# Optimization experiments

Hardware: AMD Instinct MI355X
Metric: run time of the kernel (lower is better)

## Reference

```python
import jax, jax.numpy as jnp
import numpy as np
import math

B, S, E, H, L = 32, 512, 256, 8, 2
Dh = E // H
NUM_Q, NUM_C, MAX_POS, R = 10000, 200, 512, 4


def setup_inputs() -> dict:
    key = jax.random.key(0)
    ks = jax.random.split(key, 32)
    f = lambda k, sh: (jax.random.normal(k, sh, jnp.float32) * 0.05)
    que_emb = f(ks[0], (NUM_Q + 1, E)).at[0].set(0.0)  # padding_idx=0
    inp = dict(
        pid_data=jax.random.randint(ks[1], (B, S), 0, NUM_Q + 1),
        c_data=jax.random.randint(ks[2], (B, S, R), 0, NUM_C),
        target=jax.random.randint(ks[3], (B, S), 0, 2),
        que_emb=que_emb,
        concept_emb=f(ks[4], (NUM_C, E)),
        pos_key_emb=f(ks[5], (MAX_POS, Dh)),
        pos_value_emb=f(ks[6], (MAX_POS, Dh)),
        qc_W=f(ks[7], (2 * E, E)), qc_b=jnp.zeros((E,), jnp.float32),
        lin_W=f(ks[8], (2 * E, E)), lin_b=jnp.zeros((E,), jnp.float32),
        Wq=f(ks[9], (L, E, E)), bq=jnp.zeros((L, E), jnp.float32),
        Wk=f(ks[10], (L, E, E)), bk=jnp.zeros((L, E), jnp.float32),
        Wv=f(ks[11], (L, E, E)), bv=jnp.zeros((L, E), jnp.float32),
        o1_W=f(ks[12], (2 * E, E)), o1_b=jnp.zeros((E,), jnp.float32),
        o2_W=f(ks[13], (E, E)), o2_b=jnp.zeros((E,), jnp.float32),
        o3_W=f(ks[14], (E, 1)), o3_b=jnp.zeros((1,), jnp.float32),
    )
    return inp


def _relative_attention(q_in, v_in, Wq, bq, Wk, bk, Wv, bv, pos_key_emb, pos_value_emb):
    b, s, e = q_in.shape
    proj = lambda x, W, bias: (x @ W + bias).reshape(b, s, H, Dh).transpose(0, 2, 1, 3)
    q = proj(q_in, Wq, bq)  # [b,h,s,dh]
    k = proj(q_in, Wk, bk)
    v = proj(v_in, Wv, bv)
    # relative position indices, clamped (Shaw et al. variant)
    i = jnp.arange(s)
    idxs = jnp.clip(i[:, None] - i[None, :], 0, MAX_POS - 1)  # [s,s]
    pos_k = pos_key_emb[idxs]    # [s,s,dh]
    pos_v = pos_value_emb[idxs]  # [s,s,dh]
    scores = jnp.einsum('bhid,bhjd->bhij', q, k) + jnp.einsum('bhid,ijd->bhij', q, pos_k)
    scores = scores / math.sqrt(Dh)
    # future_mask: triu with k=0 -> mask j >= i (incl. diagonal)
    causal = (i[None, :] >= i[:, None])  # [s,s] True where masked
    scores = jnp.where(causal, jnp.float32(-1e9), scores)
    p = jax.nn.softmax(scores, axis=-1)  # [b,h,i,j]
    # pad-zero trick: row i=0 of attention replaced by zeros
    p = p * (i[:, None] > 0).astype(p.dtype)
    # value = v + per-pair positional value bias
    out = jnp.einsum('bhij,bhjd->bhid', p, v) + jnp.einsum('bhij,ijd->bhid', p, pos_v)
    return out.transpose(0, 2, 1, 3).reshape(b, s, E), p


def reference(pid_data, c_data, target, que_emb, concept_emb, pos_key_emb,
              pos_value_emb, qc_W, qc_b, lin_W, lin_b, Wq, bq, Wk, bk, Wv, bv,
              o1_W, o1_b, o2_W, o2_b, o3_W, o3_b):
    qemb = que_emb[pid_data]  # [B,S,E]
    # average skill embedding; index 0 of padded table is the zero/pad row
    concept_cat = jnp.concatenate([jnp.zeros((1, E), concept_emb.dtype), concept_emb], axis=0)
    related = c_data + 1  # [B,S,R]
    cemb_sum = concept_cat[related].sum(axis=-2)  # [B,S,E]
    cnt = (related != 0).sum(axis=-1, keepdims=True)
    cnt = jnp.maximum(cnt, 1)
    cemb = cemb_sum / cnt.astype(cemb_sum.dtype)
    query = jnp.concatenate([qemb, cemb], axis=-1) @ qc_W + qc_b  # [B,S,E]
    # interaction embedding gated by response label
    lbl = target[..., None].astype(query.dtype)
    inter = jnp.concatenate([query * lbl, query * (1.0 - lbl)], axis=-1)
    inter = jax.nn.relu(inter @ lin_W + lin_b)  # [B,S,E]
    sim = jax.nn.sigmoid(jnp.einsum('bse,ce->bsc', qemb, concept_emb))
    outputs, _ = _relative_attention(query, inter, Wq[0], bq[0], Wk[0], bk[0],
                                     Wv[0], bv[0], pos_key_emb, pos_value_emb)
    for l in range(1, L):
        residual, _ = _relative_attention(outputs, inter, Wq[l], bq[l], Wk[l], bk[l],
                                          Wv[l], bv[l], pos_key_emb, pos_value_emb)
        outputs = outputs + jax.nn.relu(residual)
    h = jnp.concatenate([outputs, query], axis=-1)
    h = jax.nn.relu(h @ o1_W + o1_b)
    h = jax.nn.relu(h @ o2_W + o2_b)
    pred = jax.nn.sigmoid((h @ o3_W + o3_b).squeeze(-1))  # [B,S]
    return pred, sim
```

## Files before the change

### kernel.cpp

```cpp
#include <hip/hip_runtime.h>
#include <hip/hip_bf16.h>
#include <cmath>

#define B_   32
#define S_   512
#define E_   256
#define H_   8
#define DH_  32
#define L_   2
#define R_   4
#define NUMC_ 200
#define MAXPOS_ 512
#define MTOK (B_ * S_)

typedef __attribute__((ext_vector_type(8))) short bf16x8_t;
typedef __attribute__((ext_vector_type(4))) float f32x4_t;

__device__ inline ushort bfu(float a) {
    union { __hip_bfloat16 h; ushort u; } x; x.h = __float2bfloat16(a); return x.u;
}
__device__ inline uint pk2bf(float a, float b) {
    return (uint)bfu(a) | ((uint)bfu(b) << 16);
}
__device__ inline float bf2f(ushort u) {
    union { float f; uint u; } x; x.u = (uint)u << 16; return x.f;
}
__device__ inline __hip_bfloat16 f2bf(float a) { return __float2bfloat16(a); }

__global__ __launch_bounds__(256) void wcvt_k(
    const float* __restrict__ qcW, const float* __restrict__ linW,
    const float* __restrict__ Wq, const float* __restrict__ Wk,
    const float* __restrict__ Wv, const float* __restrict__ o1W,
    const float* __restrict__ o2W, const float* __restrict__ ce,
    __hip_bfloat16* __restrict__ wb)
{
    int i = blockIdx.x * 256 + threadIdx.x;
    float v;
    if (i < 131072) {
        int n = i >> 9, k = i & 511; v = qcW[k * 256 + n];
    } else if (i < 262144) {
        int l = i - 131072; int n = l >> 9, k = l & 511; v = linW[k * 256 + n];
    } else if (i < 524288) {
        int l2 = i - 262144; int ly = l2 >> 17; int r2 = l2 & 131071;
        int n = r2 >> 8, k = r2 & 255;
        v = (n < 256) ? Wq[ly * 65536 + k * 256 + n]
                      : Wk[ly * 65536 + k * 256 + (n - 256)];
    } else if (i < 655360) {
        int l2 = i - 524288; int n = l2 >> 8, k = l2 & 255;
        int ly = n >> 8, nn = n & 255;
        v = Wv[ly * 65536 + k * 256 + nn];
    } else if (i < 786432) {
        int l = i - 655360; int n = l >> 9, k = l & 511; v = o1W[k * 256 + n];
    } else if (i < 851968) {
        int l = i - 786432; int n = l >> 8, k = l & 255; v = o2W[k * 256 + n];
    } else {
        int l = i - 851968; int c = l >> 8, k = l & 255;
        v = (c < NUMC_) ? ce[c * 256 + k] : 0.f;
    }
    wb[i] = f2bf(v);
}

__global__ __launch_bounds__(256) void embed_k(
    const int* __restrict__ pid, const int* __restrict__ cdat,
    const float* __restrict__ qe, const float* __restrict__ ce,
    __hip_bfloat16* __restrict__ qemb, __hip_bfloat16* __restrict__ cemb)
{
    int tkn = blockIdx.x;
    int e   = threadIdx.x;
    int p = pid[tkn];
    qemb[(size_t)tkn * E_ + e] = f2bf(qe[(size_t)p * E_ + e]);
    const int* c = cdat + (size_t)tkn * R_;
    float s = 0.f;
#pragma unroll
    for (int r = 0; r < R_; ++r) s += ce[(size_t)c[r] * E_ + e];
    cemb[(size_t)tkn * E_ + e] = f2bf(s * 0.25f);
}

template<int AMODE, int EPI, int OMODE, int K, int NB>
__global__ __launch_bounds__(256) void gemm_bf_k(
    const __hip_bfloat16* __restrict__ A0, const __hip_bfloat16* __restrict__ A1,
    const int* __restrict__ lbl,
    const __hip_bfloat16* __restrict__ BT,
    const float* __restrict__ bias, const float* __restrict__ bias2,
    void* __restrict__ C0, void* __restrict__ C1, int Nstride)
{
    const int lane = threadIdx.x & 63, w = threadIdx.x >> 6;
    const int col = lane & 15, rg = lane >> 4;
    const int wr = w >> 1, wc = w & 1;
    int did = blockIdx.y * gridDim.x + blockIdx.x;
    int bm, bn;
    if (NB == 512) {
        int swz = (did & 7) * 128 + (did >> 3);
        bm = (swz >> 2) * 64; bn = (swz & 3) * 128;
    } else {
        int swz = (did & 7) * 64 + (did >> 3);
        bm = (swz >> 1) * 64; bn = (swz & 1) * 128;
    }
    const f32x4_t z4 = {0.f, 0.f, 0.f, 0.f};
    f32x4_t acc[2][4] = {{z4, z4, z4, z4}, {z4, z4, z4, z4}};
    const bf16x8_t z8 = {0, 0, 0, 0, 0, 0, 0, 0};

    int rowA[2];
    rowA[0] = bm + wr * 32 + col;
    rowA[1] = bm + wr * 32 + 16 + col;
    int lblv[2] = {0, 0};
    if (AMODE == 2) { lblv[0] = lbl[rowA[0]]; lblv[1] = lbl[rowA[1]]; }
    const int nb0 = bn + wc * 64;

    for (int k0 = 0; k0 < K; k0 += 32) {
        const int kk = k0 + 8 * rg;
        bf16x8_t af[2], bfr[4];
#pragma unroll
        for (int mt = 0; mt < 2; ++mt) {
            if (AMODE == 0) {
                af[mt] = *reinterpret_cast<const bf16x8_t*>(A0 + (size_t)rowA[mt] * K + kk);
            } else if (AMODE == 1) {
                const __hip_bfloat16* p = (kk < 256) ? (A0 + (size_t)rowA[mt] * 256 + kk)
                                                     : (A1 + (size_t)rowA[mt] * 256 + (kk - 256));
                af[mt] = *reinterpret_cast<const bf16x8_t*>(p);
            } else {
                bf16x8_t a = *reinterpret_cast<const bf16x8_t*>(A0 + (size_t)rowA[mt] * 256 + (kk & 255));
                bool first = (kk < 256);
                af[mt] = ((lblv[mt] != 0) == first) ? a : z8;
            }
        }
#pragma unroll
        for (int nt = 0; nt < 4; ++nt)
            bfr[nt] = *reinterpret_cast<const bf16x8_t*>(BT + (size_t)(nb0 + nt * 16 + col) * K + kk);

        __builtin_amdgcn_s_setprio(1);
#pragma unroll
        for (int mt = 0; mt < 2; ++mt)
#pragma unroll
        for (int nt = 0; nt < 4; ++nt)
            acc[mt][nt] = __builtin_amdgcn_mfma_f32_16x16x32_bf16(af[mt], bfr[nt], acc[mt][nt], 0, 0, 0);
        __builtin_amdgcn_s_setprio(0);
    }

#pragma unroll
    for (int mt = 0; mt < 2; ++mt)
#pragma unroll
    for (int nt = 0; nt < 4; ++nt) {
        const int n = nb0 + nt * 16 + col;
        const int mb = bm + wr * 32 + mt * 16 + 4 * rg;
        float bs = 0.f;
        if (bias) bs = (NB == 512 && n >= 256) ? bias2[n - 256] : bias[n];
        float xv[4];
#pragma unroll
        for (int r = 0; r < 4; ++r) {
            float x = acc[mt][nt][r] + bs;
            if (EPI == 1) x = fmaxf(x, 0.f);
            else if (EPI == 2) x = 1.f / (1.f + expf(-x));
            xv[r] = x;
        }
        if (OMODE == 0) {
            if (n < Nstride) {
                float* C = (float*)C0;
#pragma unroll
                for (int r = 0; r < 4; ++r)
                    C[(size_t)(mb + r) * Nstride + n] = xv[r];
            }
        } else if (OMODE == 3) {
            __hip_bfloat16* Cb = (__hip_bfloat16*)C0;
#pragma unroll
            for (int r = 0; r < 4; ++r)
                Cb[(size_t)(mb + r) * 256 + n] = f2bf(xv[r]);
        } else if (OMODE == 1) {
            __hip_bfloat16* dst = (n < 256) ? (__hip_bfloat16*)C0 : (__hip_bfloat16*)C1;
            const int nn = n & 255, hh = nn >> 5, d = nn & 31;
#pragma unroll
            for (int r = 0; r < 4; ++r) {
                int m = mb + r;
                int bh = (m >> 9) * 8 + hh;
                dst[((size_t)bh * 512 + (m & 511)) * 32 + d] = f2bf(xv[r]);
            }
        } else {
            __hip_bfloat16* dst = (n < 256) ? (__hip_bfloat16*)C0 : (__hip_bfloat16*)C1;
            const int nn = n & 255, hh = nn >> 5, d = nn & 31;
            const int bh = (mb >> 9) * 8 + hh;
            ushort4 pk;
            pk.x = bfu(xv[0]); pk.y = bfu(xv[1]); pk.z = bfu(xv[2]); pk.w = bfu(xv[3]);
            *reinterpret_cast<ushort4*>(dst + ((size_t)bh * 32 + d) * 512 + (mb & 511)) = pk;
        }
    }
}

__global__ __launch_bounds__(256) void poscvt_k(
    const float* __restrict__ posk, const float* __restrict__ posv,
    __hip_bfloat16* __restrict__ pkPad, __hip_bfloat16* __restrict__ pvT)
{
    int t = blockIdx.x * 256 + threadIdx.x;
    {
        int row = t >> 5, d = t & 31;
        int rel = row - 32;
        float v = (rel >= 0 && rel < MAXPOS_) ? posk[(size_t)rel * DH_ + d] : 0.f;
        pkPad[t] = f2bf(v);
    }
    {
        int d = t / 576, c = t - d * 576;
        int rel = c - 31;
        float v = (rel >= 0 && rel < MAXPOS_) ? posv[(size_t)rel * DH_ + d] : 0.f;
        pvT[t] = f2bf(v);
    }
}

#define QPST 38
template<int ADDREL>
__global__ __launch_bounds__(256) void attn_mfma_k(
    const __hip_bfloat16* __restrict__ Qbf, const __hip_bfloat16* __restrict__ Kbf,
    const __hip_bfloat16* __restrict__ Vt,  const __hip_bfloat16* __restrict__ pkPad,
    const __hip_bfloat16* __restrict__ pvT, __hip_bfloat16* __restrict__ outp)
{
    __shared__ __align__(16) ushort ldsA_s[4][64 * QPST];
    __shared__ __align__(16) ushort ldsP_s[4][2304];

    const int w = threadIdx.x >> 6, lane = threadIdx.x & 63;
    const int col = lane & 15, rg = lane >> 4;
    const int bh = blockIdx.x, b = bh >> 3, h = bh & 7;
    const int s = blockIdx.y * 4 + w;
    const int band = (s & 1) ? (15 - (s >> 1)) : (s >> 1);
    const int i0 = band * 32;

    ushort* ldsA = ldsA_s[w];
    ushort* ldsP = ldsP_s[w];

    {
        uint4 zz = make_uint4(0u, 0u, 0u, 0u);
        uint4* pz = reinterpret_cast<uint4*>(ldsP);
#pragma unroll
        for (int t = 0; t < 5; ++t) {
            int idx = lane + 64 * t;
            if (idx < 288) pz[idx] = zz;
        }
    }

    const __hip_bfloat16* Qb = Qbf + (size_t)bh * 512 * 32;
    const __hip_bfloat16* Kb = Kbf + (size_t)bh * 512 * 32;
    const __hip_bfloat16* Vb = Vt  + (size_t)bh * 32 * 512;

    bf16x8_t qf[2];
    qf[0] = *reinterpret_cast<const bf16x8_t*>(Qb + (size_t)(i0 + col) * 32 + 8 * rg);
    qf[1] = *reinterpret_cast<const bf16x8_t*>(Qb + (size_t)(i0 + 16 + col) * 32 + 8 * rg);

    const f32x4_t z4 = {0.f, 0.f, 0.f, 0.f};
    f32x4_t o[2][2] = {{z4, z4}, {z4, z4}};
    float lrow[2][4] = {};
    const float rscale = 0.17677669529663687f;

    for (int j0 = 0; j0 <= i0; j0 += 32) {
        bf16x8_t kf0 = *reinterpret_cast<const bf16x8_t*>(Kb + (size_t)(j0 + col) * 32 + 8 * rg);
        bf16x8_t kf1 = *reinterpret_cast<const bf16x8_t*>(Kb + (size_t)(j0 + 16 + col) * 32 + 8 * rg);
        const int prow0 = i0 - j0 + 1;
        bf16x8_t pkf[4];
#pragma unroll
        for (int rt = 0; rt < 4; ++rt)
            pkf[rt] = *reinterpret_cast<const bf16x8_t*>(
                pkPad + (size_t)(prow0 + rt * 16 + col) * 32 + 8 * rg);

        __builtin_amdgcn_s_setprio(1);
        f32x4_t sA[2][2];
        sA[0][0] = __builtin_amdgcn_mfma_f32_16x16x32_bf16(qf[0], kf0, z4, 0, 0, 0);
        sA[0][1] = __builtin_amdgcn_mfma_f32_16x16x32_bf16(qf[0], kf1, z4, 0, 0, 0);
        sA[1][0] = __builtin_amdgcn_mfma_f32_16x16x32_bf16(qf[1], kf0, z4, 0, 0, 0);
        sA[1][1] = __builtin_amdgcn_mfma_f32_16x16x32_bf16(qf[1], kf1, z4, 0, 0, 0);
        f32x4_t qp0[4], qp1[4];
#pragma unroll
        for (int rt = 0; rt < 4; ++rt) {
            qp0[rt] = __builtin_amdgcn_mfma_f32_16x16x32_bf16(qf[0], pkf[rt], z4, 0, 0, 0);
            qp1[rt] = __builtin_amdgcn_mfma_f32_16x16x32_bf16(qf[1], pkf[rt], z4, 0, 0, 0);
        }
        __builtin_amdgcn_s_setprio(0);

#pragma unroll
        for (int rt = 0; rt < 4; ++rt) {
            int xo = (rt * 16 + col) * QPST;
            uint2 wv;
            wv.x = pk2bf(qp0[rt][0], qp0[rt][1]);
            wv.y = pk2bf(qp0[rt][2], qp0[rt][3]);
            *reinterpret_cast<uint2*>(&ldsA[xo + 4 * rg]) = wv;
            wv.x = pk2bf(qp1[rt][0], qp1[rt][1]);
            wv.y = pk2bf(qp1[rt][2], qp1[rt][3]);
            *reinterpret_cast<uint2*>(&ldsA[xo + 16 + 4 * rg]) = wv;
        }

        const bool diag = (j0 == i0);
        float ev[2][2][4];
#pragma unroll
        for (int mt = 0; mt < 2; ++mt)
#pragma unroll
        for (int r = 0; r < 4; ++r) {
            const int ii = mt * 16 + 4 * rg + r;
#pragma unroll
            for (int nt = 0; nt < 2; ++nt) {
                const int jj = nt * 16 + col;
                float qpv = bf2f(ldsA[(ii - jj + 31) * QPST + ii]);
                float sc = (sA[mt][nt][r] + qpv) * rscale;
                float e = __expf(sc);
                if (diag && jj >= ii) e = 0.f;
                ev[mt][nt][r] = e;
            }
            lrow[mt][r] += ev[mt][0][r] + ev[mt][1][r];
        }

#pragma unroll
        for (int mt = 0; mt < 2; ++mt)
#pragma unroll
        for (int nt = 0; nt < 2; ++nt)
#pragma unroll
        for (int r = 0; r < 4; ++r) {
            const int ii = mt * 16 + 4 * rg + r;
            const int jj = nt * 16 + col;
            ushort pe = bfu(ev[mt][nt][r]);
            ldsA[ii * 32 + (jj ^ ((ii & 3) << 3))] = pe;
            ldsP[ii * 72 + (ii - jj + 31)] = pe;
        }

        bf16x8_t pa0 = *reinterpret_cast<const bf16x8_t*>(&ldsA[col * 32 + (8 * rg ^ ((col & 3) << 3))]);
        bf16x8_t pa1 = *reinterpret_cast<const bf16x8_t*>(&ldsA[(16 + col) * 32 + (8 * rg ^ ((col & 3) << 3))]);
        bf16x8_t vf0 = *reinterpret_cast<const bf16x8_t*>(Vb + (size_t)col * 512 + j0 + 8 * rg);
        bf16x8_t vf1 = *reinterpret_cast<const bf16x8_t*>(Vb + (size_t)(16 + col) * 512 + j0 + 8 * rg);
        bf16x8_t pr0[2], pr1[2], pv0[2], pv1[2];
#pragma unroll
        for (int ks = 0; ks < 2; ++ks) {
            pr0[ks] = *reinterpret_cast<const bf16x8_t*>(&ldsP[col * 72 + ks * 32 + 8 * rg]);
            pr1[ks] = *reinterpret_cast<const bf16x8_t*>(&ldsP[(16 + col) * 72 + ks * 32 + 8 * rg]);
            const __hip_bfloat16* pvb = pvT + (i0 - j0) + ks * 32 + 8 * rg;
            pv0[ks] = *reinterpret_cast<const bf16x8_t*>(pvb + (size_t)col * 576);
            pv1[ks] = *reinterpret_cast<const bf16x8_t*>(pvb + (size_t)(16 + col) * 576);
        }
        __builtin_amdgcn_s_setprio(1);
        o[0][0] = __builtin_amdgcn_mfma_f32_16x16x32_bf16(pa0, vf0, o[0][0], 0, 0, 0);
        o[0][1] = __builtin_amdgcn_mfma_f32_16x16x32_bf16(pa0, vf1, o[0][1], 0, 0, 0);
        o[1][0] = __builtin_amdgcn_mfma_f32_16x16x32_bf16(pa1, vf0, o[1][0], 0, 0, 0);
        o[1][1] = __builtin_amdgcn_mfma_f32_16x16x32_bf16(pa1, vf1, o[1][1], 0, 0, 0);
#pragma unroll
        for (int ks = 0; ks < 2; ++ks) {
            o[0][0] = __builtin_amdgcn_mfma_f32_16x16x32_bf16(pr0[ks], pv0[ks], o[0][0], 0, 0, 0);
            o[0][1] = __builtin_amdgcn_mfma_f32_16x16x32_bf16(pr0[ks], pv1[ks], o[0][1], 0, 0, 0);
            o[1][0] = __builtin_amdgcn_mfma_f32_16x16x32_bf16(pr1[ks], pv0[ks], o[1][0], 0, 0, 0);
            o[1][1] = __builtin_amdgcn_mfma_f32_16x16x32_bf16(pr1[ks], pv1[ks], o[1][1], 0, 0, 0);
        }
        __builtin_amdgcn_s_setprio(0);
    }

#pragma unroll
    for (int mt = 0; mt < 2; ++mt)
#pragma unroll
    for (int r = 0; r < 4; ++r) {
        float ls = lrow[mt][r];
        ls += __shfl_xor(ls, 1); ls += __shfl_xor(ls, 2);
        ls += __shfl_xor(ls, 4); ls += __shfl_xor(ls, 8);
        const int i = i0 + mt * 16 + 4 * rg + r;
        float inv = (i == 0) ? 0.f : 1.0f / ls;
        __hip_bfloat16* orow = outp + (size_t)(b * 512 + i) * 256 + h * 32;
        float v0 = o[mt][0][r] * inv;
        float v1 = o[mt][1][r] * inv;
        if (ADDREL) {
            v0 = bf2f(*(ushort*)&orow[col])      + fmaxf(v0, 0.f);
            v1 = bf2f(*(ushort*)&orow[16 + col]) + fmaxf(v1, 0.f);
        }
        orow[col]      = f2bf(v0);
        orow[16 + col] = f2bf(v1);
    }
}

__global__ __launch_bounds__(256) void final_k(
    const __hip_bfloat16* __restrict__ h, const float* __restrict__ w3,
    const float* __restrict__ b3, float* __restrict__ pred)
{
    int wv   = threadIdx.x >> 6;
    int lane = threadIdx.x & 63;
    int m = blockIdx.x * 4 + wv;
    const __hip_bfloat16* row = h + (size_t)m * E_;
    float s = 0.f;
#pragma unroll
    for (int k = lane; k < E_; k += 64) s += bf2f(*(const ushort*)&row[k]) * w3[k];
#pragma unroll
    for (int off = 32; off; off >>= 1) s += __shfl_xor(s, off);
    if (lane == 0) pred[m] = 1.f / (1.f + expf(-(s + b3[0])));
}

extern "C" void kernel_launch(void* const* d_in, const int* in_sizes, int n_in,
                              void* d_out, int out_size, void* d_ws, size_t ws_size,
                              hipStream_t stream)
{
    const int*   pid        = (const int*)d_in[0];
    const int*   cdat       = (const int*)d_in[1];
    const int*   target     = (const int*)d_in[2];
    const float* que_emb    = (const float*)d_in[3];
    const float* concept_emb= (const float*)d_in[4];
    const float* posk       = (const float*)d_in[5];
    const float* posv       = (const float*)d_in[6];
    const float* qcW        = (const float*)d_in[7];
    const float* qcb        = (const float*)d_in[8];
    const float* linW       = (const float*)d_in[9];
    const float* linb       = (const float*)d_in[10];
    const float* Wq         = (const float*)d_in[11];
    const float* bq         = (const float*)d_in[12];
    const float* Wk         = (const float*)d_in[13];
    const float* bk         = (const float*)d_in[14];
    const float* Wv         = (const float*)d_in[15];
    const float* bv         = (const float*)d_in[16];
    const float* o1W        = (const float*)d_in[17];
    const float* o1b        = (const float*)d_in[18];
    const float* o2W        = (const float*)d_in[19];
    const float* o2b        = (const float*)d_in[20];
    const float* o3W        = (const float*)d_in[21];
    const float* o3b        = (const float*)d_in[22];

    float* out  = (float*)d_out;
    float* pred = out;
    float* sim  = out + MTOK;

    __hip_bfloat16* wsb = (__hip_bfloat16*)d_ws;
    const size_t HB = (size_t)MTOK * E_;
    __hip_bfloat16* qemb  = wsb + 0 * HB;
    __hip_bfloat16* cemb  = wsb + 1 * HB;
    __hip_bfloat16* query = wsb + 2 * HB;
    __hip_bfloat16* inter = wsb + 3 * HB;
    __hip_bfloat16* qbuf  = wsb + 4 * HB;
    __hip_bfloat16* kbuf  = wsb + 5 * HB;
    __hip_bfloat16* v0    = wsb + 6 * HB;
    __hip_bfloat16* v1    = wsb + 7 * HB;
    __hip_bfloat16* outp  = wsb + 8 * HB;
    __hip_bfloat16* h1    = wsb + 9 * HB;
    __hip_bfloat16* h2    = wsb + 10 * HB;
    __hip_bfloat16* wb    = wsb + 11 * HB;
    __hip_bfloat16* qcWT  = wb;
    __hip_bfloat16* linWT = wb + 131072;
    __hip_bfloat16* wqkT  = wb + 262144;
    __hip_bfloat16* wvT   = wb + 524288;
    __hip_bfloat16* o1WT  = wb + 655360;
    __hip_bfloat16* o2WT  = wb + 786432;
    __hip_bfloat16* ceT   = wb + 851968;
    __hip_bfloat16* pkPad = wb + 917504;
    __hip_bfloat16* pvT   = pkPad + 18432;

    dim3 blk(256);
    dim3 g256(2, 256);
    dim3 g512(4, 256);
    dim3 gattn(B_ * H_, 4);

    wcvt_k<<<3584, blk, 0, stream>>>(qcW, linW, Wq, Wk, Wv, o1W, o2W, concept_emb, wb);
    embed_k<<<MTOK, blk, 0, stream>>>(pid, cdat, que_emb, concept_emb, qemb, cemb);
    poscvt_k<<<72, blk, 0, stream>>>(posk, posv, pkPad, pvT);

    gemm_bf_k<1, 0, 3, 512, 256><<<g256, blk, 0, stream>>>(qemb, cemb, nullptr, qcWT, qcb, nullptr, query, nullptr, 256);
    gemm_bf_k<2, 1, 3, 512, 256><<<g256, blk, 0, stream>>>(query, nullptr, target, linWT, linb, nullptr, inter, nullptr, 256);
    gemm_bf_k<0, 2, 0, 256, 256><<<g256, blk, 0, stream>>>(qemb, nullptr, nullptr, ceT, nullptr, nullptr, sim, nullptr, 200);
    gemm_bf_k<0, 0, 2, 256, 512><<<g512, blk, 0, stream>>>(inter, nullptr, nullptr, wvT, bv, bv + 256, v0, v1, 0);

    gemm_bf_k<0, 0, 1, 256, 512><<<g512, blk, 0, stream>>>(query, nullptr, nullptr, wqkT, bq, bk, qbuf, kbuf, 0);
    attn_mfma_k<0><<<gattn, blk, 0, stream>>>(qbuf, kbuf, v0, pkPad, pvT, outp);

    gemm_bf_k<0, 0, 1, 256, 512><<<g512, blk, 0, stream>>>(outp, nullptr, nullptr, wqkT + 131072, bq + 256, bk + 256, qbuf, kbuf, 0);
    attn_mfma_k<1><<<gattn, blk, 0, stream>>>(qbuf, kbuf, v1, pkPad, pvT, outp);

    gemm_bf_k<1, 1, 3, 512, 256><<<g256, blk, 0, stream>>>(outp, query, nullptr, o1WT, o1b, nullptr, h1, nullptr, 256);
    gemm_bf_k<0, 1, 3, 256, 256><<<g256, blk, 0, stream>>>(h1, nullptr, nullptr, o2WT, o2b, nullptr, h2, nullptr, 256);
    final_k<<<MTOK / 4, blk, 0, stream>>>(h2, o3W, o3b, pred);
}
```

Before: 349.1 us.

## Split attention key tiles across warps and vectorize embedding gather

New measurement: 365.1 us. 1.05x slower.

```diff
diff --git a/kernel.cpp b/kernel.cpp
--- a/kernel.cpp
+++ b/kernel.cpp
@@ -65,15 +65,22 @@
     const float* __restrict__ qe, const float* __restrict__ ce,
     __hip_bfloat16* __restrict__ qemb, __hip_bfloat16* __restrict__ cemb)
 {
-    int tkn = blockIdx.x;
-    int e   = threadIdx.x;
+    int tkn = blockIdx.x * 4 + (threadIdx.x >> 6);
+    int e4  = (threadIdx.x & 63) * 4;
     int p = pid[tkn];
-    qemb[(size_t)tkn * E_ + e] = f2bf(qe[(size_t)p * E_ + e]);
+    float4 q = *reinterpret_cast<const float4*>(qe + (size_t)p * E_ + e4);
+    ushort4 qo; qo.x = bfu(q.x); qo.y = bfu(q.y); qo.z = bfu(q.z); qo.w = bfu(q.w);
+    *reinterpret_cast<ushort4*>(qemb + (size_t)tkn * E_ + e4) = qo;
     const int* c = cdat + (size_t)tkn * R_;
-    float s = 0.f;
-#pragma unroll
-    for (int r = 0; r < R_; ++r) s += ce[(size_t)c[r] * E_ + e];
-    cemb[(size_t)tkn * E_ + e] = f2bf(s * 0.25f);
+    float4 s = make_float4(0.f, 0.f, 0.f, 0.f);
+#pragma unroll
+    for (int r = 0; r < R_; ++r) {
+        float4 v = *reinterpret_cast<const float4*>(ce + (size_t)c[r] * E_ + e4);
+        s.x += v.x; s.y += v.y; s.z += v.z; s.w += v.w;
+    }
+    ushort4 co; co.x = bfu(s.x * 0.25f); co.y = bfu(s.y * 0.25f);
+    co.z = bfu(s.z * 0.25f); co.w = bfu(s.w * 0.25f);
+    *reinterpret_cast<ushort4*>(cemb + (size_t)tkn * E_ + e4) = co;
 }
 
 template<int AMODE, int EPI, int OMODE, int K, int NB>
@@ -206,161 +213,196 @@
 
 #define QPST 38
 template<int ADDREL>
-__global__ __launch_bounds__(256) void attn_mfma_k(
+__global__ __launch_bounds__(256) void attn_split_k(
     const __hip_bfloat16* __restrict__ Qbf, const __hip_bfloat16* __restrict__ Kbf,
     const __hip_bfloat16* __restrict__ Vt,  const __hip_bfloat16* __restrict__ pkPad,
     const __hip_bfloat16* __restrict__ pvT, __hip_bfloat16* __restrict__ outp)
 {
-    __shared__ __align__(16) ushort ldsA_s[4][64 * QPST];
-    __shared__ __align__(16) ushort ldsP_s[4][2304];
+    __shared__ __align__(16) ushort lds_s[4][4736];
 
     const int w = threadIdx.x >> 6, lane = threadIdx.x & 63;
     const int col = lane & 15, rg = lane >> 4;
     const int bh = blockIdx.x, b = bh >> 3, h = bh & 7;
-    const int s = blockIdx.y * 4 + w;
-    const int band = (s & 1) ? (15 - (s >> 1)) : (s >> 1);
-    const int i0 = band * 32;
-
-    ushort* ldsA = ldsA_s[w];
-    ushort* ldsP = ldsP_s[w];
-
-    {
-        uint4 zz = make_uint4(0u, 0u, 0u, 0u);
-        uint4* pz = reinterpret_cast<uint4*>(ldsP);
-#pragma unroll
-        for (int t = 0; t < 5; ++t) {
-            int idx = lane + 64 * t;
-            if (idx < 288) pz[idx] = zz;
-        }
-    }
+    const int p = blockIdx.y;
+
+    ushort* ldsA = lds_s[w];
+    ushort* ldsP = lds_s[w] + 2432;
 
     const __hip_bfloat16* Qb = Qbf + (size_t)bh * 512 * 32;
     const __hip_bfloat16* Kb = Kbf + (size_t)bh * 512 * 32;
     const __hip_bfloat16* Vb = Vt  + (size_t)bh * 32 * 512;
 
-    bf16x8_t qf[2];
-    qf[0] = *reinterpret_cast<const bf16x8_t*>(Qb + (size_t)(i0 + col) * 32 + 8 * rg);
-    qf[1] = *reinterpret_cast<const bf16x8_t*>(Qb + (size_t)(i0 + 16 + col) * 32 + 8 * rg);
-
     const f32x4_t z4 = {0.f, 0.f, 0.f, 0.f};
-    f32x4_t o[2][2] = {{z4, z4}, {z4, z4}};
-    float lrow[2][4] = {};
     const float rscale = 0.17677669529663687f;
 
-    for (int j0 = 0; j0 <= i0; j0 += 32) {
-        bf16x8_t kf0 = *reinterpret_cast<const bf16x8_t*>(Kb + (size_t)(j0 + col) * 32 + 8 * rg);
-        bf16x8_t kf1 = *reinterpret_cast<const bf16x8_t*>(Kb + (size_t)(j0 + 16 + col) * 32 + 8 * rg);
-        const int prow0 = i0 - j0 + 1;
-        bf16x8_t pkf[4];
-#pragma unroll
-        for (int rt = 0; rt < 4; ++rt)
-            pkf[rt] = *reinterpret_cast<const bf16x8_t*>(
-                pkPad + (size_t)(prow0 + rt * 16 + col) * 32 + 8 * rg);
-
-        __builtin_amdgcn_s_setprio(1);
-        f32x4_t sA[2][2];
-        sA[0][0] = __builtin_amdgcn_mfma_f32_16x16x32_bf16(qf[0], kf0, z4, 0, 0, 0);
-        sA[0][1] = __builtin_amdgcn_mfma_f32_16x16x32_bf16(qf[0], kf1, z4, 0, 0, 0);
-        sA[1][0] = __builtin_amdgcn_mfma_f32_16x16x32_bf16(qf[1], kf0, z4, 0, 0, 0);
-        sA[1][1] = __builtin_amdgcn_mfma_f32_16x16x32_bf16(qf[1], kf1, z4, 0, 0, 0);
-        f32x4_t qp0[4], qp1[4];
-#pragma unroll
-        for (int rt = 0; rt < 4; ++rt) {
-            qp0[rt] = __builtin_amdgcn_mfma_f32_16x16x32_bf16(qf[0], pkf[rt], z4, 0, 0, 0);
-            qp1[rt] = __builtin_amdgcn_mfma_f32_16x16x32_bf16(qf[1], pkf[rt], z4, 0, 0, 0);
+    for (int phase = 0; phase < 2; ++phase) {
+        const int band = phase ? (15 - p) : p;
+        const int i0 = band * 32;
+        const int nT = band + 1;
+
+        {
+            uint4 zz = make_uint4(0u, 0u, 0u, 0u);
+            uint4* pz = reinterpret_cast<uint4*>(ldsP);
+#pragma unroll
+            for (int t = 0; t < 5; ++t) {
+                int idx = lane + 64 * t;
+                if (idx < 288) pz[idx] = zz;
+            }
         }
-        __builtin_amdgcn_s_setprio(0);
-
-#pragma unroll
-        for (int rt = 0; rt < 4; ++rt) {
-            int xo = (rt * 16 + col) * QPST;
-            uint2 wv;
-            wv.x = pk2bf(qp0[rt][0], qp0[rt][1]);
-            wv.y = pk2bf(qp0[rt][2], qp0[rt][3]);
-            *reinterpret_cast<uint2*>(&ldsA[xo + 4 * rg]) = wv;
-            wv.x = pk2bf(qp1[rt][0], qp1[rt][1]);
-            wv.y = pk2bf(qp1[rt][2], qp1[rt][3]);
-            *reinterpret_cast<uint2*>(&ldsA[xo + 16 + 4 * rg]) = wv;
+
+        bf16x8_t qf[2];
+        qf[0] = *reinterpret_cast<const bf16x8_t*>(Qb + (size_t)(i0 + col) * 32 + 8 * rg);
+        qf[1] = *reinterpret_cast<const bf16x8_t*>(Qb + (size_t)(i0 + 16 + col) * 32 + 8 * rg);
+
+        f32x4_t o[2][2] = {{z4, z4}, {z4, z4}};
+        float lrow[2][4] = {};
+
+        for (int t = w; t < nT; t += 4) {
+            const int j0 = t * 32;
+            bf16x8_t kf0 = *reinterpret_cast<const bf16x8_t*>(Kb + (size_t)(j0 + col) * 32 + 8 * rg);
+            bf16x8_t kf1 = *reinterpret_cast<const bf16x8_t*>(Kb + (size_t)(j0 + 16 + col) * 32 + 8 * rg);
+            const int prow0 = i0 - j0 + 1;
+            bf16x8_t pkf[4];
+#pragma unroll
+            for (int rt = 0; rt < 4; ++rt)
+                pkf[rt] = *reinterpret_cast<const bf16x8_t*>(
+                    pkPad + (size_t)(prow0 + rt * 16 + col) * 32 + 8 * rg);
+
+            __builtin_amdgcn_s_setprio(1);
+            f32x4_t sA[2][2];
+            sA[0][0] = __builtin_amdgcn_mfma_f32_16x16x32_bf16(qf[0], kf0, z4, 0, 0, 0);
+            sA[0][1] = __builtin_amdgcn_mfma_f32_16x16x32_bf16(qf[0], kf1, z4, 0, 0, 0);
+            sA[1][0] = __builtin_amdgcn_mfma_f32_16x16x32_bf16(qf[1], kf0, z4, 0, 0, 0);
+            sA[1][1] = __builtin_amdgcn_mfma_f32_16x16x32_bf16(qf[1], kf1, z4, 0, 0, 0);
+            f32x4_t qp0[4], qp1[4];
+#pragma unroll
+            for (int rt = 0; rt < 4; ++rt) {
+                qp0[rt] = __builtin_amdgcn_mfma_f32_16x16x32_bf16(qf[0], pkf[rt], z4, 0, 0, 0);
+                qp1[rt] = __builtin_amdgcn_mfma_f32_16x16x32_bf16(qf[1], pkf[rt], z4, 0, 0, 0);
+            }
+            __builtin_amdgcn_s_setprio(0);
+
+#pragma unroll
+            for (int rt = 0; rt < 4; ++rt) {
+                int xo = (rt * 16 + col) * QPST;
+                uint2 wv;
+                wv.x = pk2bf(qp0[rt][0], qp0[rt][1]);
+                wv.y = pk2bf(qp0[rt][2], qp0[rt][3]);
+                *reinterpret_cast<uint2*>(&ldsA[xo + 4 * rg]) = wv;
+                wv.x = pk2bf(qp1[rt][0], qp1[rt][1]);
+                wv.y = pk2bf(qp1[rt][2], qp1[rt][3]);
+                *reinterpret_cast<uint2*>(&ldsA[xo + 16 + 4 * rg]) = wv;
+            }
+
+            const bool diag = (j0 == i0);
+            float ev[2][2][4];
+#pragma unroll
+            for (int mt = 0; mt < 2; ++mt)
+#pragma unroll
+            for (int r = 0; r < 4; ++r) {
+                const int ii = mt * 16 + 4 * rg + r;
+#pragma unroll
+                for (int nt = 0; nt < 2; ++nt) {
+                    const int jj = nt * 16 + col;
+                    float qpv = bf2f(ldsA[(ii - jj + 31) * QPST + ii]);
+                    float sc = (sA[mt][nt][r] + qpv) * rscale;
+                    float e = __expf(sc);
+                    if (diag && jj >= ii) e = 0.f;
+                    ev[mt][nt][r] = e;
+                }
+                lrow[mt][r] += ev[mt][0][r] + ev[mt][1][r];
+            }
+
+#pragma unroll
+            for (int mt = 0; mt < 2; ++mt)
+#pragma unroll
+            for (int nt = 0; nt < 2; ++nt)
+#pragma unroll
+            for (int r = 0; r < 4; ++r) {
+                const int ii = mt * 16 + 4 * rg + r;
+                const int jj = nt * 16 + col;
+                ushort pe = bfu(ev[mt][nt][r]);
+                ldsA[ii * 32 + (jj ^ ((ii & 3) << 3))] = pe;
+                ldsP[ii * 72 + (ii - jj + 31)] = pe;
+            }
+
+            bf16x8_t pa0 = *reinterpret_cast<const bf16x8_t*>(&ldsA[col * 32 + (8 * rg ^ ((col & 3) << 3))]);
+            bf16x8_t pa1 = *reinterpret_cast<const bf16x8_t*>(&ldsA[(16 + col) * 32 + (8 * rg ^ ((col & 3) << 3))]);
+            bf16x8_t vf0 = *reinterpret_cast<const bf16x8_t*>(Vb + (size_t)col * 512 + j0 + 8 * rg);
+            bf16x8_t vf1 = *reinterpret_cast<const bf16x8_t*>(Vb + (size_t)(16 + col) * 512 + j0 + 8 * rg);
+            bf16x8_t pr0[2], pr1[2], pv0[2], pv1[2];
+#pragma unroll
+            for (int ks = 0; ks < 2; ++ks) {
+                pr0[ks] = *reinterpret_cast<const bf16x8_t*>(&ldsP[col * 72 + ks * 32 + 8 * rg]);
+                pr1[ks] = *reinterpret_cast<const bf16x8_t*>(&ldsP[(16 + col) * 72 + ks * 32 + 8 * rg]);
+                const __hip_bfloat16* pvb = pvT + (i0 - j0) + ks * 32 + 8 * rg;
+                pv0[ks] = *reinterpret_cast<const bf16x8_t*>(pvb + (size_t)col * 576);
+                pv1[ks] = *reinterpret_cast<const bf16x8_t*>(pvb + (size_t)(16 + col) * 576);
+            }
+            __builtin_amdgcn_s_setprio(1);
+            o[0][0] = __builtin_amdgcn_mfma_f32_16x16x32_bf16(pa0, vf0, o[0][0], 0, 0, 0);
+            o[0][1] = __builtin_amdgcn_mfma_f32_16x16x32_bf16(pa0, vf1, o[0][1], 0, 0, 0);
+            o[1][0] = __builtin_amdgcn_mfma_f32_16x16x32_bf16(pa1, vf0, o[1][0], 0, 0, 0);
+            o[1][1] = __builtin_amdgcn_mfma_f32_16x16x32_bf16(pa1, vf1, o[1][1], 0, 0, 0);
+#pragma unroll
+            for (int ks = 0; ks < 2; ++ks) {
+                o[0][0] = __builtin_amdgcn_mfma_f32_16x16x32_bf16(pr0[ks], pv0[ks], o[0][0], 0, 0, 0);
+                o[0][1] = __builtin_amdgcn_mfma_f32_16x16x32_bf16(pr0[ks], pv1[ks], o[0][1], 0, 0, 0);
+                o[1][0] = __builtin_amdgcn_mfma_f32_16x16x32_bf16(pr1[ks], pv0[ks], o[1][0], 0, 0, 0);
+                o[1][1] = __builtin_amdgcn_mfma_f32_16x16x32_bf16(pr1[ks], pv1[ks], o[1][1], 0, 0, 0);
+            }
+            __builtin_amdgcn_s_setprio(0);
         }
 
-        const bool diag = (j0 == i0);
-        float ev[2][2][4];
+        float* slab = reinterpret_cast<float*>(lds_s[w]);
 #pragma unroll
         for (int mt = 0; mt < 2; ++mt)
 #pragma unroll
-        for (int r = 0; r < 4; ++r) {
-            const int ii = mt * 16 + 4 * rg + r;
-#pragma unroll
-            for (int nt = 0; nt < 2; ++nt) {
-                const int jj = nt * 16 + col;
-                float qpv = bf2f(ldsA[(ii - jj + 31) * QPST + ii]);
-                float sc = (sA[mt][nt][r] + qpv) * rscale;
-                float e = __expf(sc);
-                if (diag && jj >= ii) e = 0.f;
-                ev[mt][nt][r] = e;
-            }
-            lrow[mt][r] += ev[mt][0][r] + ev[mt][1][r];
+        for (int nt = 0; nt < 2; ++nt)
+#pragma unroll
+        for (int r = 0; r < 4; ++r)
+            slab[((mt * 2 + nt) * 4 + r) * 64 + lane] = o[mt][nt][r];
+#pragma unroll
+        for (int mt = 0; mt < 2; ++mt)
+#pragma unroll
+        for (int r = 0; r < 4; ++r)
+            slab[1024 + (mt * 4 + r) * 64 + lane] = lrow[mt][r];
+        __syncthreads();
+
+        if (w < 2) {
+            float osum[2][4] = {};
+            float lsum[4] = {};
+#pragma unroll
+            for (int sw = 0; sw < 4; ++sw) {
+                const float* sl = reinterpret_cast<const float*>(lds_s[sw]);
+#pragma unroll
+                for (int nt = 0; nt < 2; ++nt)
+#pragma unroll
+                for (int r = 0; r < 4; ++r)
+                    osum[nt][r] += sl[((w * 2 + nt) * 4 + r) * 64 + lane];
+#pragma unroll
+                for (int r = 0; r < 4; ++r)
+                    lsum[r] += sl[1024 + (w * 4 + r) * 64 + lane];
+            }
+#pragma unroll
+            for (int r = 0; r < 4; ++r) {
+                float ls = lsum[r];
+                ls += __shfl_xor(ls, 1); ls += __shfl_xor(ls, 2);
+                ls += __shfl_xor(ls, 4); ls += __shfl_xor(ls, 8);
+                const int i = i0 + w * 16 + 4 * rg + r;
+                float inv = (i == 0) ? 0.f : 1.0f / ls;
+                __hip_bfloat16* orow = outp + (size_t)(b * 512 + i) * 256 + h * 32;
+                float v0 = osum[0][r] * inv;
+                float v1 = osum[1][r] * inv;
+                if (ADDREL) {
+                    v0 = bf2f(*(ushort*)&orow[col])      + fmaxf(v0, 0.f);
+                    v1 = bf2f(*(ushort*)&orow[16 + col]) + fmaxf(v1, 0.f);
+                }
+                orow[col]      = f2bf(v0);
+                orow[16 + col] = f2bf(v1);
+            }
         }
-
-#pragma unroll
-        for (int mt = 0; mt < 2; ++mt)
-#pragma unroll
-        for (int nt = 0; nt < 2; ++nt)
-#pragma unroll
-        for (int r = 0; r < 4; ++r) {
-            const int ii = mt * 16 + 4 * rg + r;
-            const int jj = nt * 16 + col;
-            ushort pe = bfu(ev[mt][nt][r]);
-            ldsA[ii * 32 + (jj ^ ((ii & 3) << 3))] = pe;
-            ldsP[ii * 72 + (ii - jj + 31)] = pe;
-        }
-
-        bf16x8_t pa0 = *reinterpret_cast<const bf16x8_t*>(&ldsA[col * 32 + (8 * rg ^ ((col & 3) << 3))]);
-        bf16x8_t pa1 = *reinterpret_cast<const bf16x8_t*>(&ldsA[(16 + col) * 32 + (8 * rg ^ ((col & 3) << 3))]);
-        bf16x8_t vf0 = *reinterpret_cast<const bf16x8_t*>(Vb + (size_t)col * 512 + j0 + 8 * rg);
-        bf16x8_t vf1 = *reinterpret_cast<const bf16x8_t*>(Vb + (size_t)(16 + col) * 512 + j0 + 8 * rg);
-        bf16x8_t pr0[2], pr1[2], pv0[2], pv1[2];
-#pragma unroll
-        for (int ks = 0; ks < 2; ++ks) {
-            pr0[ks] = *reinterpret_cast<const bf16x8_t*>(&ldsP[col * 72 + ks * 32 + 8 * rg]);
-            pr1[ks] = *reinterpret_cast<const bf16x8_t*>(&ldsP[(16 + col) * 72 + ks * 32 + 8 * rg]);
-            const __hip_bfloat16* pvb = pvT + (i0 - j0) + ks * 32 + 8 * rg;
-            pv0[ks] = *reinterpret_cast<const bf16x8_t*>(pvb + (size_t)col * 576);
-            pv1[ks] = *reinterpret_cast<const bf16x8_t*>(pvb + (size_t)(16 + col) * 576);
-        }
-        __builtin_amdgcn_s_setprio(1);
-        o[0][0] = __builtin_amdgcn_mfma_f32_16x16x32_bf16(pa0, vf0, o[0][0], 0, 0, 0);
-        o[0][1] = __builtin_amdgcn_mfma_f32_16x16x32_bf16(pa0, vf1, o[0][1], 0, 0, 0);
-        o[1][0] = __builtin_amdgcn_mfma_f32_16x16x32_bf16(pa1, vf0, o[1][0], 0, 0, 0);
-        o[1][1] = __builtin_amdgcn_mfma_f32_16x16x32_bf16(pa1, vf1, o[1][1], 0, 0, 0);
-#pragma unroll
-        for (int ks = 0; ks < 2; ++ks) {
-            o[0][0] = __builtin_amdgcn_mfma_f32_16x16x32_bf16(pr0[ks], pv0[ks], o[0][0], 0, 0, 0);
-            o[0][1] = __builtin_amdgcn_mfma_f32_16x16x32_bf16(pr0[ks], pv1[ks], o[0][1], 0, 0, 0);
-            o[1][0] = __builtin_amdgcn_mfma_f32_16x16x32_bf16(pr1[ks], pv0[ks], o[1][0], 0, 0, 0);
-            o[1][1] = __builtin_amdgcn_mfma_f32_16x16x32_bf16(pr1[ks], pv1[ks], o[1][1], 0, 0, 0);
-        }
-        __builtin_amdgcn_s_setprio(0);
-    }
-
-#pragma unroll
-    for (int mt = 0; mt < 2; ++mt)
-#pragma unroll
-    for (int r = 0; r < 4; ++r) {
-        float ls = lrow[mt][r];
-        ls += __shfl_xor(ls, 1); ls += __shfl_xor(ls, 2);
-        ls += __shfl_xor(ls, 4); ls += __shfl_xor(ls, 8);
-        const int i = i0 + mt * 16 + 4 * rg + r;
-        float inv = (i == 0) ? 0.f : 1.0f / ls;
-        __hip_bfloat16* orow = outp + (size_t)(b * 512 + i) * 256 + h * 32;
-        float v0 = o[mt][0][r] * inv;
-        float v1 = o[mt][1][r] * inv;
-        if (ADDREL) {
-            v0 = bf2f(*(ushort*)&orow[col])      + fmaxf(v0, 0.f);
-            v1 = bf2f(*(ushort*)&orow[16 + col]) + fmaxf(v1, 0.f);
-        }
-        orow[col]      = f2bf(v0);
-        orow[16 + col] = f2bf(v1);
+        __syncthreads();
     }
 }
 
@@ -439,10 +481,10 @@
     dim3 blk(256);
     dim3 g256(2, 256);
     dim3 g512(4, 256);
-    dim3 gattn(B_ * H_, 4);
+    dim3 gattn(B_ * H_, 8);
 
     wcvt_k<<<3584, blk, 0, stream>>>(qcW, linW, Wq, Wk, Wv, o1W, o2W, concept_emb, wb);
-    embed_k<<<MTOK, blk, 0, stream>>>(pid, cdat, que_emb, concept_emb, qemb, cemb);
+    embed_k<<<MTOK / 4, blk, 0, stream>>>(pid, cdat, que_emb, concept_emb, qemb, cemb);
     poscvt_k<<<72, blk, 0, stream>>>(posk, posv, pkPad, pvT);
 
     gemm_bf_k<1, 0, 3, 512, 256><<<g256, blk, 0, stream>>>(qemb, cemb, nullptr, qcWT, qcb, nullptr, query, nullptr, 256);
@@ -451,10 +493,10 @@
     gemm_bf_k<0, 0, 2, 256, 512><<<g512, blk, 0, stream>>>(inter, nullptr, nullptr, wvT, bv, bv + 256, v0, v1, 0);
 
     gemm_bf_k<0, 0, 1, 256, 512><<<g512, blk, 0, stream>>>(query, nullptr, nullptr, wqkT, bq, bk, qbuf, kbuf, 0);
-    attn_mfma_k<0><<<gattn, blk, 0, stream>>>(qbuf, kbuf, v0, pkPad, pvT, outp);
+    attn_split_k<0><<<gattn, blk, 0, stream>>>(qbuf, kbuf, v0, pkPad, pvT, outp);
 
     gemm_bf_k<0, 0, 1, 256, 512><<<g512, blk, 0, stream>>>(outp, nullptr, nullptr, wqkT + 131072, bq + 256, bk + 256, qbuf, kbuf, 0);
-    attn_mfma_k<1><<<gattn, blk, 0, stream>>>(qbuf, kbuf, v1, pkPad, pvT, outp);
+    attn_split_k<1><<<gattn, blk, 0, stream>>>(qbuf, kbuf, v1, pkPad, pvT, outp);
 
     gemm_bf_k<1, 1, 3, 512, 256><<<g256, blk, 0, stream>>>(outp, query, nullptr, o1WT, o1b, nullptr, h1, nullptr, 256);
     gemm_bf_k<0, 1, 3, 256, 256><<<g256, blk, 0, stream>>>(h1, nullptr, nullptr, o2WT, o2b, nullptr, h2, nullptr, 256);
```
